# Kernel tuning notes

Measured on AMD Instinct MI355X. Metric: run time of the kernel, lower is better.

## Reference

```python
import jax, jax.numpy as jnp
import numpy as np

K = 3          # kernel_size
PAD = 1        # padding for offset conv and deform conv
UPS = 2        # ConvTranspose2d stride
EPS = 1e-5     # BatchNorm eps


def _conv2d(x, w, b, pad):
    y = jax.lax.conv_general_dilated(x, w, (1, 1), [(pad, pad), (pad, pad)],
                                     dimension_numbers=('NCHW', 'OIHW', 'NCHW'))
    return y + b[None, :, None, None]


def _deform_conv(x, offsets, w, b):
    # torchvision DeformConv2d semantics, stride=1, pad=1, dilation=1
    B, C, H, W = x.shape
    KK = K * K
    off = offsets.reshape(B, KK, 2, H, W)  # [:, kk, 0]=dy, [:, kk, 1]=dx
    ki, kj = jnp.meshgrid(jnp.arange(K), jnp.arange(K), indexing='ij')
    py = (jnp.arange(H) - PAD)[None, None, :, None] + ki.ravel()[None, :, None, None] + off[:, :, 0]
    px = (jnp.arange(W) - PAD)[None, None, None, :] + kj.ravel()[None, :, None, None] + off[:, :, 1]
    y0f = jnp.floor(py); x0f = jnp.floor(px)
    ly = py - y0f; lx = px - x0f
    y0 = y0f.astype(jnp.int32); x0 = x0f.astype(jnp.int32)
    xf = x.reshape(B, C, H * W)

    def corner(yy, xx, wgt):
        valid = (yy >= 0) & (yy < H) & (xx >= 0) & (xx < W)
        idx = jnp.clip(yy, 0, H - 1) * W + jnp.clip(xx, 0, W - 1)      # [B,KK,H,W]
        v = jax.vmap(lambda f, i: f[:, i])(xf, idx)                     # [B,C,KK,H,W]
        return v * (wgt * valid)[:, None]

    s = (corner(y0, x0, (1 - ly) * (1 - lx)) + corner(y0, x0 + 1, (1 - ly) * lx)
         + corner(y0 + 1, x0, ly * (1 - lx)) + corner(y0 + 1, x0 + 1, ly * lx))
    out = jnp.einsum('bckhw,ock->bohw', s, w.reshape(w.shape[0], C, KK))
    return out + b[None, :, None, None]


def _conv_transpose(x, w, b):
    # torch ConvTranspose2d(stride=UPS, padding=0); torch weight is [C_in, C_out, K, K]
    wf = jnp.flip(jnp.transpose(w, (1, 0, 2, 3)), (2, 3))
    y = jax.lax.conv_general_dilated(x, wf, (1, 1), [(K - 1, K - 1)] * 2,
                                     lhs_dilation=(UPS, UPS),
                                     dimension_numbers=('NCHW', 'OIHW', 'NCHW'))
    return y + b[None, :, None, None]


def setup_inputs() -> dict:
    key = jax.random.key(0)
    ks = jax.random.split(key, 8)
    B, Cin, Cout, H, W = 16, 64, 128, 64, 64
    s = 0.05
    return {
        'x': jax.random.normal(ks[0], (B, Cin, H, W), jnp.float32),
        'w_off': jax.random.normal(ks[1], (2 * K * K, Cin, K, K), jnp.float32) * s,
        'b_off': jax.random.normal(ks[2], (2 * K * K,), jnp.float32) * s,
        'w_def': jax.random.normal(ks[3], (Cout, Cin, K, K), jnp.float32) * s,
        'b_def': jax.random.normal(ks[4], (Cout,), jnp.float32) * s,
        'w_up': jax.random.normal(ks[5], (Cout, Cout, K, K), jnp.float32) * s,
        'b_up': jax.random.normal(ks[6], (Cout,), jnp.float32) * s,
        'gamma': jnp.ones((Cout,), jnp.float32),
        'beta': jnp.zeros((Cout,), jnp.float32),
    }


def reference(x, w_off, b_off, w_def, b_def, w_up, b_up, gamma, beta):
    offsets = _conv2d(x, w_off, b_off, PAD)
    feats = _deform_conv(x, offsets, w_def, b_def)
    y = _conv_transpose(feats, w_up, b_up)
    # BatchNorm2d (training mode, biased batch stats) + ReLU
    mu = jnp.mean(y, axis=(0, 2, 3), keepdims=True)
    var = jnp.var(y, axis=(0, 2, 3), keepdims=True)
    yn = (y - mu) * jax.lax.rsqrt(var + EPS)
    yn = yn * gamma[None, :, None, None] + beta[None, :, None, None]
    return jax.nn.relu(yn)
```

## Files before the change

### kernel.cpp

```cpp
#include <hip/hip_runtime.h>
#include <math.h>

#define PADC 1
#define CIN  64
#define COUT 128
#define IH   64
#define IW   64
#define NB   16
#define OYX  129
#define OXP  136
#define NOFF 18
#define SPO  (OYX * OYX)
#define BNEPS 1e-5f
#define NBLK_CT (NB * 65)

typedef __attribute__((ext_vector_type(8))) short bf16x8;
typedef __attribute__((ext_vector_type(4))) float f32x4;

static __device__ __forceinline__ unsigned short f2bf(float f) {
    unsigned int b = __float_as_uint(f);
    unsigned int r = (b + 0x7FFFu + ((b >> 16) & 1u)) >> 16;
    return (unsigned short)r;
}
static __device__ __forceinline__ float bf2f(unsigned short u) {
    return __uint_as_float((unsigned int)u << 16);
}

__global__ __launch_bounds__(256) void k_pre(
    const float* __restrict__ x, const float* __restrict__ w_def,
    const float* __restrict__ w_up, const float* __restrict__ w_off,
    unsigned short* __restrict__ xt, unsigned short* __restrict__ WDF,
    unsigned short* __restrict__ WB, unsigned short* __restrict__ WOF)
{
    __shared__ unsigned short t[64][66];
    const int tid = threadIdx.x;
    if (blockIdx.x < 1024) {
        const int h = blockIdx.x & 63, b = blockIdx.x >> 6;
        const int w = tid & 63, cq = tid >> 6;
        #pragma unroll
        for (int p = 0; p < 16; ++p) {
            const int c = p * 4 + cq;
            t[w][c] = f2bf(x[((size_t)((b * 64 + c) * 64) + h) * 64 + w]);
        }
        __syncthreads();
        const int w2 = tid >> 2, q = tid & 3;
        unsigned int pk[8];
        #pragma unroll
        for (int m = 0; m < 8; ++m)
            pk[m] = (unsigned int)t[w2][q * 16 + 2 * m] | ((unsigned int)t[w2][q * 16 + 2 * m + 1] << 16);
        uint4* dst = (uint4*)(xt + ((size_t)((b * 64 + h) * 64) + w2) * 64 + q * 16);
        dst[0] = uint4{pk[0], pk[1], pk[2], pk[3]};
        dst[1] = uint4{pk[4], pk[5], pk[6], pk[7]};
        return;
    }
    int idx = (blockIdx.x - 1024) * 256 + tid;
    if (idx < 73728) {
        const int j = idx & 7;
        const int n = (idx >> 3) & 127;
        const int g = idx >> 10;
        const int kg = g & 3, ks = (g >> 2) & 1, kk = g >> 3;
        const int c = ks * 32 + kg * 8 + j;
        WDF[idx] = f2bf(w_def[(n * CIN + c) * 9 + kk]);
    }
    const int i2 = idx - 73728;
    if (i2 >= 0 && i2 < 147456) {
        const int j = i2 & 7;
        const int n = (i2 >> 3) & 127;
        int ky, kx, ci;
        if (i2 < 65536) {
            const int k = (i2 >> 10) * 8 + j;
            ky = (k >> 8) ? 0 : 2;
            kx = ((k >> 7) & 1) ? 0 : 2;
            ci = k & 127;
        } else if (i2 < 98304) {
            const int k = ((i2 - 65536) >> 10) * 8 + j;
            ky = 1;
            kx = (k >> 7) ? 0 : 2;
            ci = k & 127;
        } else if (i2 < 131072) {
            const int k = ((i2 - 98304) >> 10) * 8 + j;
            ky = (k >> 7) ? 0 : 2;
            kx = 1;
            ci = k & 127;
        } else {
            const int k = ((i2 - 131072) >> 10) * 8 + j;
            ky = 1; kx = 1;
            ci = k & 127;
        }
        WB[i2] = f2bf(w_up[((ci * COUT + n) * 3 + ky) * 3 + kx]);
    }
    const int i3 = idx - 221184;
    if (i3 >= 0 && i3 < 18432) {
        const int j = i3 & 7;
        const int n = (i3 >> 3) & 31;
        const int g = i3 >> 8;
        const int kg = g & 3, s = g >> 2;
        const int c  = (s & 1) * 32 + kg * 8 + j;
        const int kk = s >> 1;
        const int ki = kk / 3, kj = kk - 3 * ki;
        WOF[i3] = (n < NOFF) ? f2bf(w_off[((n * CIN + c) * 3 + ki) * 3 + kj]) : (unsigned short)0;
    }
}

__global__ __launch_bounds__(64, 4) void k_offset_mfma(
    const unsigned short* __restrict__ xt, const unsigned short* __restrict__ WOF,
    const float* __restrict__ b_off, float* __restrict__ offs2)
{
    const int l  = threadIdx.x;
    const int ml = l & 15;
    const int kg = l >> 4;
    const int q  = blockIdx.x & 3;
    const int h  = (blockIdx.x >> 2) & 63;
    const int b  = blockIdx.x >> 8;
    const int w  = q * 16 + ml;
    const unsigned short* xb = xt + (size_t)b * (IH * IW * CIN);

    const f32x4 fz = {0.f, 0.f, 0.f, 0.f};
    f32x4 acc0 = fz, acc1 = fz;

    #pragma unroll 1
    for (int s = 0; s < 18; ++s) {
        const int kk = s >> 1;
        const int ki = kk / 3, kj = kk - 3 * ki;
        const int c0 = (s & 1) * 32 + kg * 8;
        const int yy = h - PADC + ki;
        const int xx = w - PADC + kj;
        const bf16x8 b0 = *(const bf16x8*)(WOF + (size_t)(((s * 4 + kg) * 32 + ml) * 8));
        const bf16x8 b1 = *(const bf16x8*)(WOF + (size_t)(((s * 4 + kg) * 32 + 16 + ml) * 8));
        bf16x8 a = {0, 0, 0, 0, 0, 0, 0, 0};
        if (yy >= 0 && yy < IH && xx >= 0 && xx < IW)
            a = *(const bf16x8*)(xb + (size_t)((yy * IW + xx) * CIN) + c0);
        acc0 = __builtin_amdgcn_mfma_f32_16x16x32_bf16(a, b0, acc0, 0, 0, 0);
        acc1 = __builtin_amdgcn_mfma_f32_16x16x32_bf16(a, b1, acc1, 0, 0, 0);
    }
    #pragma unroll
    for (int nt = 0; nt < 2; ++nt) {
        const int oc = nt * 16 + ml;
        if (oc < NOFF) {
            const float bias = b_off[oc];
            const f32x4 av = nt ? acc1 : acc0;
            #pragma unroll
            for (int j = 0; j < 4; ++j) {
                const int wd = q * 16 + kg * 4 + j;
                offs2[((size_t)((b * IH + h) * IW) + wd) * NOFF + oc] = av[j] + bias;
            }
        }
    }
}

__global__ __launch_bounds__(64, 4) void k_deform_mfma(
    const unsigned short* __restrict__ xt, const float* __restrict__ offs2,
    const unsigned short* __restrict__ WDF, const float* __restrict__ b_def,
    unsigned short* __restrict__ feats_bf)
{
    const int l  = threadIdx.x;
    const int ml = l & 15;
    const int kg = l >> 4;
    const int q  = blockIdx.x & 3;
    const int h  = (blockIdx.x >> 2) & 63;
    const int b  = blockIdx.x >> 8;
    const int w  = q * 16 + ml;

    const unsigned short* xb = xt + (size_t)b * (IH * IW * CIN);

    float2 dd[9];
    {
        const float* op = offs2 + ((size_t)((b * IH + h) * IW) + w) * NOFF;
        #pragma unroll
        for (int kk = 0; kk < 9; ++kk)
            dd[kk] = *(const float2*)(op + 2 * kk);
    }

    const f32x4 fz = {0.f, 0.f, 0.f, 0.f};
    f32x4 acc[8];
    #pragma unroll
    for (int nt = 0; nt < 8; ++nt) acc[nt] = fz;

    #pragma unroll
    for (int kk = 0; kk < 9; ++kk) {
        const int ki = kk / 3, kj = kk - 3 * ki;
        const float py = (float)(h - PADC + ki) + dd[kk].x;
        const float px = (float)(w - PADC + kj) + dd[kk].y;
        const float y0f = floorf(py), x0f = floorf(px);
        const float ly = py - y0f, lx = px - x0f;
        const int y0 = (int)y0f, x0 = (int)x0f;
        const float wy[2] = {1.f - ly, ly};
        const float wx[2] = {1.f - lx, lx};
        int   cidx[4];
        float cwgt[4];
        #pragma unroll
        for (int cy = 0; cy < 2; ++cy)
            #pragma unroll
            for (int cx = 0; cx < 2; ++cx) {
                const int yy = y0 + cy, xx = x0 + cx;
                const bool v = (yy >= 0) & (yy < IH) & (xx >= 0) & (xx < IW);
                cidx[cy * 2 + cx] = v ? ((yy * IW + xx) * CIN) : 0;
                cwgt[cy * 2 + cx] = v ? (wy[cy] * wx[cx]) : 0.f;
            }
        #pragma unroll
        for (int ks = 0; ks < 2; ++ks) {
            const int c0 = ks * 32 + kg * 8;
            uint4 cv[4];
            #pragma unroll
            for (int cp = 0; cp < 4; ++cp)
                cv[cp] = *(const uint4*)(xb + cidx[cp] + c0);
            float sf[8] = {0.f, 0.f, 0.f, 0.f, 0.f, 0.f, 0.f, 0.f};
            #pragma unroll
            for (int cp = 0; cp < 4; ++cp) {
                const float wg = cwgt[cp];
                const unsigned int u0 = cv[cp].x, u1 = cv[cp].y, u2 = cv[cp].z, u3 = cv[cp].w;
                sf[0] += wg * __uint_as_float(u0 << 16);
                sf[1] += wg * __uint_as_float(u0 & 0xFFFF0000u);
                sf[2] += wg * __uint_as_float(u1 << 16);
                sf[3] += wg * __uint_as_float(u1 & 0xFFFF0000u);
                sf[4] += wg * __uint_as_float(u2 << 16);
                sf[5] += wg * __uint_as_float(u2 & 0xFFFF0000u);
                sf[6] += wg * __uint_as_float(u3 << 16);
                sf[7] += wg * __uint_as_float(u3 & 0xFFFF0000u);
            }
            union { unsigned short us[8]; bf16x8 v; } pa;
            #pragma unroll
            for (int j = 0; j < 8; ++j) pa.us[j] = f2bf(sf[j]);
            #pragma unroll
            for (int half = 0; half < 2; ++half) {
                bf16x8 bfr[4];
                #pragma unroll
                for (int nn = 0; nn < 4; ++nn)
                    bfr[nn] = *(const bf16x8*)(WDF + ((size_t)((kk * 8 + ks * 4 + kg) * 128) + (half * 4 + nn) * 16 + ml) * 8);
                #pragma unroll
                for (int nn = 0; nn < 4; ++nn)
                    acc[half * 4 + nn] = __builtin_amdgcn_mfma_f32_16x16x32_bf16(pa.v, bfr[nn], acc[half * 4 + nn], 0, 0, 0);
            }
        }
    }
    #pragma unroll
    for (int nt = 0; nt < 8; ++nt) {
        const int o = nt * 16 + ml;
        const float bias = b_def[o];
        #pragma unroll
        for (int j = 0; j < 4; ++j) {
            const int wd = q * 16 + kg * 4 + j;
            feats_bf[((size_t)((b * IH + h) * IW) + wd) * COUT + o] = f2bf(acc[nt][j] + bias);
        }
    }
}

__global__ __launch_bounds__(256) void k_convT_mfma(
    const unsigned short* __restrict__ feats_bf, const unsigned short* __restrict__ WB,
    unsigned short* __restrict__ y_bf, float* __restrict__ partials)
{
    __shared__ __align__(16) char smem[33792];

    const int tid = threadIdx.x;
    const int l   = tid & 63;
    const int wv  = tid >> 6;
    const int ml  = l & 15;
    const int kg  = l >> 4;
    const int blk = blockIdx.x;
    const int t   = blk % 65;
    const int b   = blk / 65;

    for (int r = 0; r < 2; ++r) {
        char* dstbase = smem + r * 16896;
        const int iy = t - 1 + r;
        if (iy < 0 || iy > 63) {
            for (int i = tid; i < 1056; i += 256)
                *(uint4*)(dstbase + i * 16) = uint4{0, 0, 0, 0};
        } else {
            const unsigned short* src = feats_bf + (size_t)(b * IH + iy) * (IW * COUT);
            for (int i = tid; i < 1024; i += 256) {
                const uint4 v = *(const uint4*)(src + i * 8);
                const int G = 16 + i;
                const int phys = G ^ ((G >> 4) & 7);
                *(uint4*)(dstbase + phys * 16) = v;
            }
            if (tid < 32) {
                const int G = (tid < 16) ? tid : (1024 + tid);
                const int phys = G ^ ((G >> 4) & 7);
                *(uint4*)(dstbase + phys * 16) = uint4{0, 0, 0, 0};
            }
        }
    }
    __syncthreads();

    const int n0 = wv * 32;
    const f32x4 fz = {0.f, 0.f, 0.f, 0.f};
    float sacc[2] = {0.f, 0.f}, qacc[2] = {0.f, 0.f};

    #pragma unroll 1
    for (int p = 0; p < 2; ++p) {
        if (p == 1 && t == 64) break;
        const int oy = 2 * t + p;
        const unsigned short* segG0 = WB + (p ? 65536 : 0);
        const unsigned short* segG1 = WB + (p ? 131072 : 98304);
        const int nK0 = p ? 8 : 16;
        const int nK1 = p ? 4 : 8;

        f32x4 acc0[5][2], acc1[4][2];
        #pragma unroll
        for (int m = 0; m < 5; ++m) { acc0[m][0] = fz; acc0[m][1] = fz; }
        #pragma unroll
        for (int m = 0; m < 4; ++m) { acc1[m][0] = fz; acc1[m][1] = fz; }

        for (int ks = 0; ks < nK0; ++ks) {
            const int kk   = ks * 32 + kg * 8;
            const int slot = p ? 1 : (kk >> 8);
            const int kb   = (kk & 255) >> 3;
            const bf16x8 b0 = *(const bf16x8*)(segG0 + ((ks * 4 + kg) * 128 + n0 + ml) * 8);
            const bf16x8 b1 = *(const bf16x8*)(segG0 + ((ks * 4 + kg) * 128 + n0 + 16 + ml) * 8);
            #pragma unroll
            for (int mt = 0; mt < 5; ++mt) {
                int tx = mt * 16 + ml; if (tx > 64) tx = 64;
                const int G = tx * 16 + kb;
                const int phys = G ^ ((G >> 4) & 7);
                const bf16x8 a = *(const bf16x8*)(smem + slot * 16896 + phys * 16);
                acc0[mt][0] = __builtin_amdgcn_mfma_f32_16x16x32_bf16(a, b0, acc0[mt][0], 0, 0, 0);
                acc0[mt][1] = __builtin_amdgcn_mfma_f32_16x16x32_bf16(a, b1, acc0[mt][1], 0, 0, 0);
            }
        }
        for (int ks = 0; ks < nK1; ++ks) {
            const int kk   = ks * 32 + kg * 8;
            const int slot = p ? 1 : (kk >> 7);
            const int kb   = (kk & 127) >> 3;
            const bf16x8 b0 = *(const bf16x8*)(segG1 + ((ks * 4 + kg) * 128 + n0 + ml) * 8);
            const bf16x8 b1 = *(const bf16x8*)(segG1 + ((ks * 4 + kg) * 128 + n0 + 16 + ml) * 8);
            #pragma unroll
            for (int mt = 0; mt < 4; ++mt) {
                const int tx = mt * 16 + ml;
                const int G = 16 + tx * 16 + kb;
                const int phys = G ^ ((G >> 4) & 7);
                const bf16x8 a = *(const bf16x8*)(smem + slot * 16896 + phys * 16);
                acc1[mt][0] = __builtin_amdgcn_mfma_f32_16x16x32_bf16(a, b0, acc1[mt][0], 0, 0, 0);
                acc1[mt][1] = __builtin_amdgcn_mfma_f32_16x16x32_bf16(a, b1, acc1[mt][1], 0, 0, 0);
            }
        }

        #pragma unroll
        for (int nt = 0; nt < 2; ++nt) {
            const int co = n0 + nt * 16 + ml;
            unsigned int* drow32 = (unsigned int*)(y_bf + ((size_t)(b * COUT + co) * OYX + oy) * OXP);
            #pragma unroll
            for (int mt = 0; mt < 4; ++mt) {
                unsigned int pk[4];
                #pragma unroll
                for (int j = 0; j < 4; ++j) {
                    const float ve = acc0[mt][nt][j];
                    const float vo = acc1[mt][nt][j];
                    pk[j] = (unsigned int)f2bf(ve) | ((unsigned int)f2bf(vo) << 16);
                    sacc[nt] += ve + vo;
                    qacc[nt] += ve * ve + vo * vo;
                }
                *(uint4*)(drow32 + mt * 16 + kg * 4) = uint4{pk[0], pk[1], pk[2], pk[3]};
            }
            if (kg == 0) {
                const float ve = acc0[4][nt][0];
                drow32[64] = (unsigned int)f2bf(ve);
                sacc[nt] += ve;
                qacc[nt] += ve * ve;
            }
        }
    }

    #pragma unroll
    for (int nt = 0; nt < 2; ++nt) {
        float ss = sacc[nt], qq = qacc[nt];
        ss += __shfl_xor(ss, 16, 64); qq += __shfl_xor(qq, 16, 64);
        ss += __shfl_xor(ss, 32, 64); qq += __shfl_xor(qq, 32, 64);
        if (kg == 0) {
            float* pp = partials + ((size_t)blk * COUT + n0 + nt * 16 + ml) * 2;
            pp[0] = ss; pp[1] = qq;
        }
    }
}

__global__ __launch_bounds__(256) void k_bn_final(const float* __restrict__ partials,
                                                  float* __restrict__ stats)
{
    const int c = blockIdx.x;
    const int tid = threadIdx.x;
    float s = 0.f, q = 0.f;
    for (int i = tid; i < NBLK_CT; i += 256) {
        const float* pp = partials + ((size_t)i * COUT + c) * 2;
        s += pp[0]; q += pp[1];
    }
    __shared__ float rs[256], rq[256];
    rs[tid] = s; rq[tid] = q;
    __syncthreads();
    for (int off = 128; off > 0; off >>= 1) {
        if (tid < off) { rs[tid] += rs[tid + off]; rq[tid] += rq[tid + off]; }
        __syncthreads();
    }
    if (tid == 0) {
        const float n = (float)(NB * SPO);
        const float mean = rs[0] / n;
        const float var  = rq[0] / n - mean * mean;
        stats[c] = mean;
        stats[COUT + c] = rsqrtf(var + BNEPS);
    }
}

__global__ __launch_bounds__(256) void k_bn_apply(
    const unsigned short* __restrict__ y_bf, float* __restrict__ y,
    const float* __restrict__ stats,
    const float* __restrict__ gamma, const float* __restrict__ beta)
{
    const int v = blockIdx.x * 256 + threadIdx.x;
    const int rid = v / 17;
    const int c   = v - rid * 17;
    const int co  = (rid / OYX) & (COUT - 1);
    const float mean = stats[co], rstd = stats[COUT + co];
    const float ga = gamma[co], be = beta[co];
    const int ox0 = c * 8;

    const uint4 u = *(const uint4*)(y_bf + (size_t)rid * OXP + ox0);
    const unsigned int uu[4] = {u.x, u.y, u.z, u.w};
    float* dst = y + (size_t)rid * OYX + ox0;
    const int nv = (c < 16) ? 8 : 1;
    #pragma unroll
    for (int m = 0; m < 4; ++m) {
        float v0 = bf2f((unsigned short)(uu[m] & 0xFFFFu));
        float v1 = bf2f((unsigned short)(uu[m] >> 16));
        v0 = fmaxf((v0 - mean) * rstd * ga + be, 0.f);
        v1 = fmaxf((v1 - mean) * rstd * ga + be, 0.f);
        if (2 * m < nv)     dst[2 * m]     = v0;
        if (2 * m + 1 < nv) dst[2 * m + 1] = v1;
    }
}

extern "C" void kernel_launch(void* const* d_in, const int* in_sizes, int n_in,
                              void* d_out, int out_size, void* d_ws, size_t ws_size,
                              hipStream_t stream)
{
    const float* x     = (const float*)d_in[0];
    const float* w_off = (const float*)d_in[1];
    const float* b_off = (const float*)d_in[2];
    const float* w_def = (const float*)d_in[3];
    const float* b_def = (const float*)d_in[4];
    const float* w_up  = (const float*)d_in[5];
    const float* b_up  = (const float*)d_in[6];  (void)b_up;
    const float* gamma = (const float*)d_in[7];
    const float* beta  = (const float*)d_in[8];
    float* y = (float*)d_out;

    float* ws       = (float*)d_ws;
    float* stats    = ws;
    float* partials = stats + 256;
    float* offs2    = partials + 528384;
    unsigned short* xt       = (unsigned short*)(offs2 + 1179648);
    unsigned short* WDF      = xt + 4194304;
    unsigned short* feats_bf = WDF + 73728;
    unsigned short* WB       = feats_bf + 8388608;
    unsigned short* WOF      = WB + 147456;
    unsigned short* y_bf     = WOF + 18432;

    k_pre          <<<dim3(1960),   dim3(256), 0, stream>>>(x, w_def, w_up, w_off, xt, WDF, WB, WOF);
    k_offset_mfma  <<<dim3(4096),   dim3(64),  0, stream>>>(xt, WOF, b_off, offs2);
    k_deform_mfma  <<<dim3(4096),   dim3(64),  0, stream>>>(xt, offs2, WDF, b_def, feats_bf);
    k_convT_mfma   <<<dim3(NBLK_CT),dim3(256), 0, stream>>>(feats_bf, WB, y_bf, partials);
    k_bn_final     <<<dim3(128),    dim3(256), 0, stream>>>(partials, stats);
    k_bn_apply     <<<dim3(17544),  dim3(256), 0, stream>>>(y_bf, y, stats, gamma, beta);
}
```

Measured before the change: 161.7 us.

## Merge deform-conv waves into 256-thread blocks sharing double-buffered LDS weights

The deformable conv kernel now runs four waves per block, each covering one quarter of an image row. Per-tap weight slices are staged into a double-buffered LDS array, with the next slice prefetched through registers. The goal is to replace redundant per-wave global or L2 weight fetches with shared LDS reads. The cost is 32 KB of LDS per block, which can limit occupancy, plus a block-wide barrier on every tap.

```diff
diff --git a/kernel.cpp b/kernel.cpp
--- a/kernel.cpp
+++ b/kernel.cpp
@@ -148,20 +148,33 @@
     }
 }
 
-__global__ __launch_bounds__(64, 4) void k_deform_mfma(
+__global__ __launch_bounds__(256, 4) void k_deform_mfma(
     const unsigned short* __restrict__ xt, const float* __restrict__ offs2,
     const unsigned short* __restrict__ WDF, const float* __restrict__ b_def,
     unsigned short* __restrict__ feats_bf)
 {
-    const int l  = threadIdx.x;
-    const int ml = l & 15;
-    const int kg = l >> 4;
-    const int q  = blockIdx.x & 3;
-    const int h  = (blockIdx.x >> 2) & 63;
-    const int b  = blockIdx.x >> 8;
-    const int w  = q * 16 + ml;
+    __shared__ __align__(16) unsigned short wlds[2][8192];
+
+    const int tid = threadIdx.x;
+    const int q   = tid >> 6;
+    const int l   = tid & 63;
+    const int ml  = l & 15;
+    const int kg  = l >> 4;
+    const int h   = blockIdx.x & 63;
+    const int b   = blockIdx.x >> 6;
+    const int w   = q * 16 + ml;
 
     const unsigned short* xb = xt + (size_t)b * (IH * IW * CIN);
+
+    uint4 st[4];
+    {
+        const uint4* s0 = (const uint4*)(WDF);
+        #pragma unroll
+        for (int i = 0; i < 4; ++i) ((uint4*)wlds[0])[tid + i * 256] = s0[tid + i * 256];
+        const uint4* s1 = (const uint4*)(WDF + 8192);
+        #pragma unroll
+        for (int i = 0; i < 4; ++i) st[i] = s1[tid + i * 256];
+    }
 
     float2 dd[9];
     {
@@ -176,8 +189,11 @@
     #pragma unroll
     for (int nt = 0; nt < 8; ++nt) acc[nt] = fz;
 
+    __syncthreads();
+
     #pragma unroll
     for (int kk = 0; kk < 9; ++kk) {
+        const int cur = kk & 1;
         const int ki = kk / 3, kj = kk - 3 * ki;
         const float py = (float)(h - PADC + ki) + dd[kk].x;
         const float px = (float)(w - PADC + kj) + dd[kk].y;
@@ -226,13 +242,24 @@
                 bf16x8 bfr[4];
                 #pragma unroll
                 for (int nn = 0; nn < 4; ++nn)
-                    bfr[nn] = *(const bf16x8*)(WDF + ((size_t)((kk * 8 + ks * 4 + kg) * 128) + (half * 4 + nn) * 16 + ml) * 8);
+                    bfr[nn] = *(const bf16x8*)(&wlds[cur][(((ks * 4 + kg) * 128) + (half * 4 + nn) * 16 + ml) * 8]);
                 #pragma unroll
                 for (int nn = 0; nn < 4; ++nn)
                     acc[half * 4 + nn] = __builtin_amdgcn_mfma_f32_16x16x32_bf16(pa.v, bfr[nn], acc[half * 4 + nn], 0, 0, 0);
             }
         }
-    }
+        if (kk < 8) {
+            #pragma unroll
+            for (int i = 0; i < 4; ++i) ((uint4*)wlds[1 - cur])[tid + i * 256] = st[i];
+            if (kk < 7) {
+                const uint4* sn = (const uint4*)(WDF + (size_t)(kk + 2) * 8192);
+                #pragma unroll
+                for (int i = 0; i < 4; ++i) st[i] = sn[tid + i * 256];
+            }
+            __syncthreads();
+        }
+    }
+
     #pragma unroll
     for (int nt = 0; nt < 8; ++nt) {
         const int o = nt * 16 + ml;
@@ -455,7 +482,7 @@
 
     k_pre          <<<dim3(1960),   dim3(256), 0, stream>>>(x, w_def, w_up, w_off, xt, WDF, WB, WOF);
     k_offset_mfma  <<<dim3(4096),   dim3(64),  0, stream>>>(xt, WOF, b_off, offs2);
-    k_deform_mfma  <<<dim3(4096),   dim3(64),  0, stream>>>(xt, offs2, WDF, b_def, feats_bf);
+    k_deform_mfma  <<<dim3(1024),   dim3(256), 0, stream>>>(xt, offs2, WDF, b_def, feats_bf);
     k_convT_mfma   <<<dim3(NBLK_CT),dim3(256), 0, stream>>>(feats_bf, WB, y_bf, partials);
     k_bn_final     <<<dim3(128),    dim3(256), 0, stream>>>(partials, stats);
     k_bn_apply     <<<dim3(17544),  dim3(256), 0, stream>>>(y_bf, y, stats, gamma, beta);
```

Measured after the change: 180.4 us. 1.12x slower.
